# Kernel tuning notes

Hardware: AMD Instinct MI355X
Metric: run time of the kernel (lower is better)

Reference implementation:

```python
import jax, jax.numpy as jnp
import numpy as np
from jax.scipy.special import digamma

# dims: B batch, N tokens, D ambient input dim, H heads, HD head ambient dim, DS spatial per head
B, N, D, H = 8, 1024, 512, 8
HD = D // H          # 64
DS = HD - 1          # 63
EPS = 1e-7
SCALE = 1.0 / np.sqrt(HD)
CURVATURE = -1.0     # k = -curvature = 1


def setup_inputs() -> dict:
    key = jax.random.key(0)
    ks = jax.random.split(key, 4)
    # points on the Lorentz hyperboloid: t = sqrt(||x_s||^2 + 1)
    x_s = jax.random.normal(ks[0], (B, N, D - 1), dtype=jnp.float32) * 0.5
    x_t = jnp.sqrt(jnp.sum(x_s * x_s, -1, keepdims=True) + 1.0)
    x = jnp.concatenate([x_t, x_s], -1)
    init = lambda k, sh: jax.random.normal(k, sh, dtype=jnp.float32) * (1.0 / np.sqrt(D))
    Wq = init(ks[1], (H, D, DS)); Wk = init(ks[2], (H, D, DS)); Wv = init(ks[3], (H, D, DS))
    bq = jnp.zeros((H, DS), jnp.float32); bk = jnp.zeros((H, DS), jnp.float32); bv = jnp.zeros((H, DS), jnp.float32)
    return {"x": x, "Wq": Wq, "bq": bq, "Wk": Wk, "bk": bk, "Wv": Wv, "bv": bv}


def lorentz_fc(x, W, b):
    # LorentzFC per head, vectorized over heads: spatial z = Wx+b, time from constraint
    z = jnp.einsum('bnd,hde->bhne', x, W) + b[None, :, None, :]   # [B,H,N,DS]
    t = jnp.sqrt(jnp.sum(z * z, -1, keepdims=True) + 1.0)
    return jnp.concatenate([t, z], -1)                            # [B,H,N,HD]


def lorentz_inner(q, k):
    time = jnp.einsum('bhni,bhmi->bhnm', q[..., :1], k[..., :1])
    space = jnp.einsum('bhnd,bhmd->bhnm', q[..., 1:], k[..., 1:])
    return -time + space


def logmap0(v):
    t, vs = v[..., :1], v[..., 1:]
    d = jnp.arccosh(jnp.maximum(t, 1.0 + EPS))
    denom = jnp.sqrt(jnp.maximum(t * t - 1.0, EPS))
    us = (d / denom) * vs
    return jnp.concatenate([jnp.zeros_like(t), us], -1)


def expmap0(u):
    us = u[..., 1:]
    r = jnp.sqrt(jnp.maximum(jnp.sum(us * us, -1, keepdims=True), EPS * EPS))
    t = jnp.cosh(r)
    xs = (jnp.sinh(r) / r) * us
    return jnp.concatenate([t, xs], -1)


def reference(x, Wq, bq, Wk, bk, Wv, bv):
    q = lorentz_fc(x, Wq, bq)
    k = lorentz_fc(x, Wk, bk)
    v = lorentz_fc(x, Wv, bv)
    scores = lorentz_inner(q, k) * SCALE            # [B,H,N,N]
    attn = jax.nn.softmax(scores, axis=-1)
    v_tan = logmap0(v)                              # [B,H,N,HD], time comp = 0
    out_tan = jnp.einsum('bhnm,bhmd->bhnd', attn, v_tan)
    out = expmap0(out_tan)                          # [B,H,N,HD]
    # curvature-aware log-radius head concat
    s = jnp.exp(0.5 * (digamma(jnp.asarray(H * DS / 2.0)) - digamma(jnp.asarray(DS / 2.0))))
    invK = 1.0 / CURVATURE                          # -1
    t_h = out[..., 0]                               # [B,H,N]
    u_h = out[..., 1:]                              # [B,H,N,DS]
    u_tilde = s * u_h
    sum_term = jnp.sum(t_h * t_h + invK, axis=1)    # [B,N]
    t_prime = jnp.sqrt(jnp.maximum(s * s * sum_term - invK, 1e-8))
    u_concat = jnp.transpose(u_tilde, (0, 2, 1, 3)).reshape(B, N, H * DS)
    return jnp.concatenate([t_prime[..., None], u_concat], -1)   # [B,N,1+H*DS]
```

## Files before the change

### kernel.cpp

```cpp
#include <hip/hip_runtime.h>
#include <math.h>

#define B_ 8
#define N_ 1024
#define D_ 512
#define H_ 8
#define HD_ 64
#define DS_ 63
#define SCALE_ 0.125f
#define EPS_ 1e-7f
#define KT_ 64

typedef short bf16x8 __attribute__((ext_vector_type(8)));
typedef float f32x16 __attribute__((ext_vector_type(16)));

typedef const __attribute__((address_space(1))) unsigned int* gas_ptr;
typedef __attribute__((address_space(3))) unsigned int* las_ptr;

__device__ inline ushort f2bf(float f) {
    uint u = __float_as_uint(f);
    uint r = (u + 0x7FFFu + ((u >> 16) & 1u)) >> 16;
    return (ushort)r;
}

__global__ void prep_kernel(const float* __restrict__ x,
                            const float* __restrict__ Wq, const float* __restrict__ Wk,
                            const float* __restrict__ Wv,
                            ushort* __restrict__ xb, ushort* __restrict__ Wt) {
    __shared__ float til[64 * 65];
    const int bid = blockIdx.x;
    if (bid < 4096) {
        int i = bid * 256 + threadIdx.x;
        float4 v = ((const float4*)x)[i];
        ushort4 o;
        o.x = f2bf(v.x); o.y = f2bf(v.y); o.z = f2bf(v.z); o.w = f2bf(v.w);
        ((ushort4*)xb)[i] = o;
    } else {
        const int b2 = bid - 4096;
        const int g = b2 >> 3, kbase = (b2 & 7) * 64;
        const int mat = g >> 3, h = g & 7;
        const float* W = (mat == 0) ? Wq : (mat == 1) ? Wk : Wv;
        const float* src = W + (size_t)h * D_ * DS_ + (size_t)kbase * DS_;
        for (int i = threadIdx.x; i < 64 * DS_; i += 256) {
            int k = i / DS_, e = i - k * DS_;
            til[k * 65 + e] = src[i];
        }
        __syncthreads();
        for (int i = threadIdx.x; i < 64 * 64; i += 256) {
            int e = i >> 6, kk = i & 63;
            float v = (e < DS_) ? til[kk * 65 + e] : 0.f;
            Wt[((size_t)g * 64 + e) * D_ + kbase + kk] = f2bf(v);
        }
    }
}

__global__ __launch_bounds__(256, 4)
void proj5_kernel(const ushort* __restrict__ Xb, const ushort* __restrict__ Wt,
                  const float* __restrict__ bq, const float* __restrict__ bk,
                  const float* __restrict__ bv,
                  ushort* __restrict__ Qo, ushort* __restrict__ Ko,
                  ushort* __restrict__ Vto)
{
    __shared__ char smem[34816];

    const int tid = threadIdx.x;
    const int wid = tid >> 6, lane = tid & 63;
    const int lm = lane & 31, g = lane >> 5;
    const int wr = wid & 1, wg = wid >> 1;
    const int R0 = blockIdx.x * 128;
    const int grp0 = blockIdx.y * 2;
    const int mat = grp0 >> 3;

    char* As = smem;
    char* Bs = smem + 16384;
    const ushort* Wg = Wt + (size_t)grp0 * 64 * D_;

    f32x16 acc00 = {0.f}, acc01 = {0.f}, acc10 = {0.f}, acc11 = {0.f};
    const int asw = (lm & 7) << 4;

    for (int t = 0; t < 8; t++) {
        __syncthreads();
#pragma unroll
        for (int it = 0; it < 4; it++) {
            int ci = it * 256 + tid;
            int row = ci >> 3, cb = (ci & 7) * 16;
            const char* src = (const char*)(Xb + (size_t)(R0 + row) * D_ + t * KT_)
                              + (cb ^ ((row & 7) << 4));
            __builtin_amdgcn_global_load_lds((gas_ptr)src,
                (las_ptr)(As + it * 4096 + wid * 1024), 16, 0, 0);
        }
#pragma unroll
        for (int it = 0; it < 4; it++) {
            int ci = it * 256 + tid;
            int row = ci >> 3, cb = (ci & 7) * 16;
            const char* src = (const char*)(Wg + (size_t)row * D_ + t * KT_)
                              + (cb ^ ((row & 7) << 4));
            __builtin_amdgcn_global_load_lds((gas_ptr)src,
                (las_ptr)(Bs + it * 4096 + wid * 1024), 16, 0, 0);
        }
        __syncthreads();
#pragma unroll
        for (int c = 0; c < 4; c++) {
            int kb = (c * 32 + g * 16) ^ asw;
            bf16x8 a0 = *(const bf16x8*)(As + (wr * 64 + lm) * 128 + kb);
            bf16x8 a1 = *(const bf16x8*)(As + (wr * 64 + 32 + lm) * 128 + kb);
            bf16x8 b0 = *(const bf16x8*)(Bs + (wg * 64 + lm) * 128 + kb);
            bf16x8 b1 = *(const bf16x8*)(Bs + (wg * 64 + 32 + lm) * 128 + kb);
            acc00 = __builtin_amdgcn_mfma_f32_32x32x16_bf16(a0, b0, acc00, 0, 0, 0);
            acc01 = __builtin_amdgcn_mfma_f32_32x32x16_bf16(a0, b1, acc01, 0, 0, 0);
            acc10 = __builtin_amdgcn_mfma_f32_32x32x16_bf16(a1, b0, acc10, 0, 0, 0);
            acc11 = __builtin_amdgcn_mfma_f32_32x32x16_bf16(a1, b1, acc11, 0, 0, 0);
        }
    }
    __syncthreads();

    float* zs   = (float*)smem;
    float* tval = (float*)(smem + 33280);
    float* cval = tval + 128;
    const float* bptr = (mat == 0) ? bq : (mat == 1) ? bk : bv;
    const int b = R0 >> 10, n0 = R0 & (N_ - 1);

    for (int pass = 0; pass < 2; pass++) {
        const int h = (grp0 + pass) & 7;
        if (pass) __syncthreads();
        if (wg == pass) {
            float ba = (lm < DS_) ? bptr[h * DS_ + lm] : 0.f;
            float bb = (lm + 32 < DS_) ? bptr[h * DS_ + lm + 32] : 0.f;
#pragma unroll
            for (int r = 0; r < 16; r++) {
                int rm = (r & 3) + 8 * (r >> 2) + 4 * g;
                zs[(wr * 64 + rm) * 65 + lm]           = acc00[r] + ba;
                zs[(wr * 64 + rm) * 65 + 32 + lm]      = acc01[r] + bb;
                zs[(wr * 64 + 32 + rm) * 65 + lm]      = acc10[r] + ba;
                zs[(wr * 64 + 32 + rm) * 65 + 32 + lm] = acc11[r] + bb;
            }
        }
        __syncthreads();
        if (tid < 128) {
            float ss = 0.f;
            for (int e = 0; e < DS_; e++) { float v = zs[tid * 65 + e]; ss += v * v; }
            float t = sqrtf(ss + 1.f);
            float w0, coef;
            if (mat == 0)      { w0 = -t * SCALE_; coef = SCALE_; }
            else if (mat == 1) { w0 =  t;          coef = 1.f; }
            else {
                float tc = fmaxf(t, 1.f + EPS_);
                float d  = acoshf(tc);
                float dn = sqrtf(fmaxf(t * t - 1.f, EPS_));
                w0 = 0.f; coef = d / dn;
            }
            tval[tid] = w0; cval[tid] = coef;
        }
        __syncthreads();

        const int bh = b * H_ + h;
        if (mat == 2) {
            for (int i = tid; i < 128 * 64; i += 256) {
                int e = i >> 7, nl = i & 127;
                float val = (e == 0) ? 1.0f : cval[nl] * zs[nl * 65 + e - 1];
                Vto[((size_t)bh * 64 + e) * N_ + n0 + nl] = f2bf(val);
            }
        } else {
            ushort* dst = (mat == 0) ? Qo : Ko;
            for (int i = tid; i < 128 * 64; i += 256) {
                int rr = i >> 6, e = i & 63;
                float val = (e == 0) ? tval[rr] : cval[rr] * zs[rr * 65 + e - 1];
                dst[((size_t)bh * N_ + n0 + rr) * 64 + e] = f2bf(val);
            }
        }
    }
}

__global__ __launch_bounds__(512, 2)
void attn6_kernel(const ushort* __restrict__ Q, const ushort* __restrict__ K,
                  const ushort* __restrict__ Vt, float* __restrict__ out,
                  float* __restrict__ TS, float sconst)
{
    __shared__ char lds[32768];

    const int tid  = threadIdx.x;
    const int wid  = tid >> 6;
    const int lane = tid & 63;
    const int lm = lane & 31, g = lane >> 5;

    const int bid = blockIdx.x;
    const int bh  = (bid >> 5) * 8 + (bid & 7);
    const int R0  = ((bid >> 3) & 3) * 256;
    const int qrow = R0 + wid * 32 + lm;

    bf16x8 qf[4];
    const ushort* qptr = Q + (((size_t)bh) * N_ + qrow) * 64 + g * 8;
#pragma unroll
    for (int c = 0; c < 4; c++)
        qf[c] = *(const bf16x8*)(qptr + c * 16);

    f32x16 acc0 = {0.f}, acc1 = {0.f};

    const ushort* kg = K  + ((size_t)bh) * N_ * 64;
    const ushort* vg = Vt + ((size_t)bh) * 64 * N_;

    auto stage = [&](int buf, int kt) {
        int row = tid >> 3, cb = (tid & 7) << 4;
        int sw = (row & 7) << 4;
        const char* srck = (const char*)(kg + (size_t)(kt + row) * 64) + (cb ^ sw);
        __builtin_amdgcn_global_load_lds((gas_ptr)srck,
            (las_ptr)(lds + buf * 8192 + wid * 1024), 16, 0, 0);
        const char* srcv = (const char*)(vg + (size_t)row * N_ + kt) + (cb ^ sw);
        __builtin_amdgcn_global_load_lds((gas_ptr)srcv,
            (las_ptr)(lds + 16384 + buf * 8192 + wid * 1024), 16, 0, 0);
    };

    stage(0, 0);
    for (int t = 0; t < 16; t++) {
        __syncthreads();
        if (t < 15) stage((t + 1) & 1, (t + 1) * KT_);
        const int cur = t & 1;
        char* kbase = lds + cur * 8192;
        char* vbase = lds + 16384 + cur * 8192;

#pragma unroll
        for (int sub = 0; sub < 2; sub++) {
            f32x16 st = {0.f};
            const int krow = sub * 32 + lm;
            const int ksw  = (krow & 7) << 4;
            __builtin_amdgcn_s_setprio(1);
#pragma unroll
            for (int c = 0; c < 4; c++) {
                bf16x8 kf = *(const bf16x8*)(kbase + krow * 128 + ((g * 16 + c * 32) ^ ksw));
                st = __builtin_amdgcn_mfma_f32_32x32x16_bf16(kf, qf[c], st, 0, 0, 0);
            }
            __builtin_amdgcn_s_setprio(0);
            float p[16];
#pragma unroll
            for (int rr = 0; rr < 16; rr++)
                p[rr] = __expf(st[rr]);
            union { uint u[8]; bf16x8 v[2]; } pu;
#pragma unroll
            for (int j = 0; j < 8; j++)
                pu.u[j] = __builtin_amdgcn_perm(__float_as_uint(p[2 * j + 1]),
                                                __float_as_uint(p[2 * j]), 0x07060302);
            __builtin_amdgcn_s_setprio(1);
#pragma unroll
            for (int c = 0; c < 2; c++) {
#pragma unroll
                for (int dh = 0; dh < 2; dh++) {
                    const int vrow = dh * 32 + lm;
                    const int vsw  = (vrow & 7) << 4;
                    const int colb = sub * 64 + 8 * g + 32 * c;
                    union { uint2 u2[2]; bf16x8 v; } uu;
                    uu.u2[0] = *(const uint2*)(vbase + vrow * 128 + ( colb       ^ vsw));
                    uu.u2[1] = *(const uint2*)(vbase + vrow * 128 + ((colb + 16) ^ vsw));
                    if (dh == 0)
                        acc0 = __builtin_amdgcn_mfma_f32_32x32x16_bf16(uu.v, pu.v[c], acc0, 0, 0, 0);
                    else
                        acc1 = __builtin_amdgcn_mfma_f32_32x32x16_bf16(uu.v, pu.v[c], acc1, 0, 0, 0);
                }
            }
            __builtin_amdgcn_s_setprio(0);
        }
    }

    float draw = acc0[0];
    float doth = __shfl_xor(draw, 32);
    float den  = (g == 0) ? draw : doth;
    if (g == 0) acc0[0] = 0.f;

    float invd = 1.f / den;
    float ss = 0.f;
#pragma unroll
    for (int j = 0; j < 16; j++) {
        acc0[j] *= invd; acc1[j] *= invd;
        ss += acc0[j] * acc0[j] + acc1[j] * acc1[j];
    }
    ss += __shfl_xor(ss, 32);
    float rr = sqrtf(fmaxf(ss, 1e-14f));
    float t  = coshf(rr);
    float coef = sconst * sinhf(rr) / rr;

    const int b = bh >> 3, h = bh & 7;
    const size_t ob = ((size_t)b * N_ + qrow) * 505 + (size_t)h * DS_;
#pragma unroll
    for (int j = 0; j < 16; j++) {
        int d = (j & 3) + 8 * (j >> 2) + 4 * g;
        if (d >= 1) out[ob + d] = coef * acc0[j];
        out[ob + d + 32] = coef * acc1[j];
    }
    if (g == 0) TS[((size_t)bh) * N_ + qrow] = t;
}

__global__ void tprime_kernel(const float* __restrict__ TS, float* __restrict__ out,
                              float sconst)
{
    int idx = blockIdx.x * 256 + threadIdx.x;
    if (idx >= B_ * N_) return;
    int b = idx >> 10, n = idx & (N_ - 1);
    float sum = 0.f;
#pragma unroll
    for (int h = 0; h < H_; h++) {
        float t = TS[((size_t)(b * H_ + h)) * N_ + n];
        sum += t * t - 1.f;
    }
    float tp = sqrtf(fmaxf(sconst * sconst * sum + 1.f, 1e-8f));
    out[(size_t)idx * 505] = tp;
}

static double digamma_(double x) {
    double r = 0.0;
    while (x < 20.0) { r -= 1.0 / x; x += 1.0; }
    double f = 1.0 / (x * x);
    return r + log(x) - 0.5 / x - f * (1.0 / 12.0 - f * (1.0 / 120.0 - f * (1.0 / 252.0)));
}

extern "C" void kernel_launch(void* const* d_in, const int* in_sizes, int n_in,
                              void* d_out, int out_size, void* d_ws, size_t ws_size,
                              hipStream_t stream) {
    const float* x  = (const float*)d_in[0];
    const float* Wq = (const float*)d_in[1];
    const float* bq = (const float*)d_in[2];
    const float* Wk = (const float*)d_in[3];
    const float* bk = (const float*)d_in[4];
    const float* Wv = (const float*)d_in[5];
    const float* bv = (const float*)d_in[6];
    float* out = (float*)d_out;

    const size_t QKV = (size_t)B_ * H_ * N_ * 64;
    ushort* Qd  = (ushort*)d_ws;
    ushort* Kd  = Qd + QKV;
    ushort* Vtd = Kd + QKV;
    ushort* Xb  = Vtd + QKV;
    ushort* Wtd = Xb + (size_t)B_ * N_ * D_;
    float*  TS  = (float*)(Wtd + (size_t)24 * 64 * D_);

    const float sconst = (float)exp(0.5 * (digamma_(H_ * DS_ / 2.0) - digamma_(DS_ / 2.0)));

    prep_kernel<<<4096 + 192, 256, 0, stream>>>(x, Wq, Wk, Wv, Xb, Wtd);
    proj5_kernel<<<dim3(64, 12), 256, 0, stream>>>(Xb, Wtd, bq, bk, bv, Qd, Kd, Vtd);
    attn6_kernel<<<256, 512, 0, stream>>>(Qd, Kd, Vtd, out, TS, sconst);
    tprime_kernel<<<(B_ * N_ + 255) / 256, 256, 0, stream>>>(TS, out, sconst);
}
```

Measured before the change: 69.83 us.

## Fold t-prime reduction into attention via atomics; use exp2 with log2e-scaled Q

Removes the separate tprime kernel launch. The attention kernel now accumulates t*t-1 per token with atomics, and the last head to arrive, detected by an atomic counter, writes t'. The accumulators are zeroed by extra blocks in the prep kernel. Separately, Q is pre-scaled by log2(e) so the softmax exponent can use exp2f instead of __expf. The change adds atomic traffic and fences at the end of attention, and makes the float summation order nondeterministic.

After: 162.5 us. +132.7%, slower.

```diff
diff --git a/kernel.cpp b/kernel.cpp
--- a/kernel.cpp
+++ b/kernel.cpp
@@ -8,6 +8,7 @@
 #define HD_ 64
 #define DS_ 63
 #define SCALE_ 0.125f
+#define LOG2E_ 1.4426950408889634f
 #define EPS_ 1e-7f
 #define KT_ 64
 
@@ -26,7 +27,8 @@
 __global__ void prep_kernel(const float* __restrict__ x,
                             const float* __restrict__ Wq, const float* __restrict__ Wk,
                             const float* __restrict__ Wv,
-                            ushort* __restrict__ xb, ushort* __restrict__ Wt) {
+                            ushort* __restrict__ xb, ushort* __restrict__ Wt,
+                            float* __restrict__ tacc, uint* __restrict__ tcnt) {
     __shared__ float til[64 * 65];
     const int bid = blockIdx.x;
     if (bid < 4096) {
@@ -35,7 +37,7 @@
         ushort4 o;
         o.x = f2bf(v.x); o.y = f2bf(v.y); o.z = f2bf(v.z); o.w = f2bf(v.w);
         ((ushort4*)xb)[i] = o;
-    } else {
+    } else if (bid < 4288) {
         const int b2 = bid - 4096;
         const int g = b2 >> 3, kbase = (b2 & 7) * 64;
         const int mat = g >> 3, h = g & 7;
@@ -51,6 +53,10 @@
             float v = (e < DS_) ? til[kk * 65 + e] : 0.f;
             Wt[((size_t)g * 64 + e) * D_ + kbase + kk] = f2bf(v);
         }
+    } else {
+        int i = (bid - 4288) * 256 + threadIdx.x;
+        tacc[i] = 0.f;
+        tcnt[i] = 0u;
     }
 }
 
@@ -141,8 +147,9 @@
             for (int e = 0; e < DS_; e++) { float v = zs[tid * 65 + e]; ss += v * v; }
             float t = sqrtf(ss + 1.f);
             float w0, coef;
-            if (mat == 0)      { w0 = -t * SCALE_; coef = SCALE_; }
-            else if (mat == 1) { w0 =  t;          coef = 1.f; }
+            if (mat == 0) {
+                w0 = -t * (SCALE_ * LOG2E_); coef = SCALE_ * LOG2E_;
+            } else if (mat == 1) { w0 = t; coef = 1.f; }
             else {
                 float tc = fmaxf(t, 1.f + EPS_);
                 float d  = acoshf(tc);
@@ -172,9 +179,10 @@
 }
 
 __global__ __launch_bounds__(512, 2)
-void attn6_kernel(const ushort* __restrict__ Q, const ushort* __restrict__ K,
+void attn7_kernel(const ushort* __restrict__ Q, const ushort* __restrict__ K,
                   const ushort* __restrict__ Vt, float* __restrict__ out,
-                  float* __restrict__ TS, float sconst)
+                  float* __restrict__ tacc, uint* __restrict__ tcnt,
+                  float sconst)
 {
     __shared__ char lds[32768];
 
@@ -233,7 +241,7 @@
             float p[16];
 #pragma unroll
             for (int rr = 0; rr < 16; rr++)
-                p[rr] = __expf(st[rr]);
+                p[rr] = exp2f(st[rr]);
             union { uint u[8]; bf16x8 v[2]; } pu;
 #pragma unroll
             for (int j = 0; j < 8; j++)
@@ -285,23 +293,19 @@
         if (d >= 1) out[ob + d] = coef * acc0[j];
         out[ob + d + 32] = coef * acc1[j];
     }
-    if (g == 0) TS[((size_t)bh) * N_ + qrow] = t;
-}
-
-__global__ void tprime_kernel(const float* __restrict__ TS, float* __restrict__ out,
-                              float sconst)
-{
-    int idx = blockIdx.x * 256 + threadIdx.x;
-    if (idx >= B_ * N_) return;
-    int b = idx >> 10, n = idx & (N_ - 1);
-    float sum = 0.f;
-#pragma unroll
-    for (int h = 0; h < H_; h++) {
-        float t = TS[((size_t)(b * H_ + h)) * N_ + n];
-        sum += t * t - 1.f;
-    }
-    float tp = sqrtf(fmaxf(sconst * sconst * sum + 1.f, 1e-8f));
-    out[(size_t)idx * 505] = tp;
+
+    if (g == 0) {
+        int idx = b * N_ + qrow;
+        atomicAdd(&tacc[idx], t * t - 1.0f);
+        __threadfence();
+        uint old = atomicAdd(&tcnt[idx], 1u);
+        if (old == H_ - 1) {
+            __threadfence();
+            float sum = atomicAdd(&tacc[idx], 0.0f);
+            float tp = sqrtf(fmaxf(sconst * sconst * sum + 1.0f, 1e-8f));
+            out[(size_t)idx * 505] = tp;
+        }
+    }
 }
 
 static double digamma_(double x) {
@@ -324,17 +328,17 @@
     float* out = (float*)d_out;
 
     const size_t QKV = (size_t)B_ * H_ * N_ * 64;
-    ushort* Qd  = (ushort*)d_ws;
-    ushort* Kd  = Qd + QKV;
-    ushort* Vtd = Kd + QKV;
-    ushort* Xb  = Vtd + QKV;
-    ushort* Wtd = Xb + (size_t)B_ * N_ * D_;
-    float*  TS  = (float*)(Wtd + (size_t)24 * 64 * D_);
+    ushort* Qd   = (ushort*)d_ws;
+    ushort* Kd   = Qd + QKV;
+    ushort* Vtd  = Kd + QKV;
+    ushort* Xb   = Vtd + QKV;
+    ushort* Wtd  = Xb + (size_t)B_ * N_ * D_;
+    float*  tacc = (float*)(Wtd + (size_t)24 * 64 * D_);
+    uint*   tcnt = (uint*)(tacc + B_ * N_);
 
     const float sconst = (float)exp(0.5 * (digamma_(H_ * DS_ / 2.0) - digamma_(DS_ / 2.0)));
 
-    prep_kernel<<<4096 + 192, 256, 0, stream>>>(x, Wq, Wk, Wv, Xb, Wtd);
+    prep_kernel<<<4096 + 192 + 32, 256, 0, stream>>>(x, Wq, Wk, Wv, Xb, Wtd, tacc, tcnt);
     proj5_kernel<<<dim3(64, 12), 256, 0, stream>>>(Xb, Wtd, bq, bk, bv, Qd, Kd, Vtd);
-    attn6_kernel<<<256, 512, 0, stream>>>(Qd, Kd, Vtd, out, TS, sconst);
-    tprime_kernel<<<(B_ * N_ + 255) / 256, 256, 0, stream>>>(TS, out, sconst);
-}
+    attn7_kernel<<<256, 512, 0, stream>>>(Qd, Kd, Vtd, out, tacc, tcnt, sconst);
+}
```
